# Kernel tuning notes

Hardware: AMD Instinct MI355X
Metric: run time of the kernel (lower is better)

The kernel has to match this reference:

```python
import jax, jax.numpy as jnp
import numpy as np

N, M, D = 16384, 1024, 32


def setup_inputs() -> dict:
    key = jax.random.key(0)
    k1, k2 = jax.random.split(key)
    x = jax.random.normal(k1, (N, D), dtype=jnp.float32)
    centers = jax.random.normal(k2, (M, D), dtype=jnp.float32)
    sigma = jnp.ones((M, D), dtype=jnp.float32)  # get_sigma_ones(s=1.0)
    return {"x": x, "centers": centers, "sigma": sigma}


def reference(x, centers, sigma):
    # Gaussian RBF kernel: exp(-0.5 * delta^T invCov delta) / sqrt((2pi)^D det(S))
    d = x.shape[1]
    s2 = sigma ** 2  # (M, D)
    # invCovMat: inverse of per-center diagonal covariance -> diag(1/s2)
    invCov = jnp.eye(d, dtype=x.dtype) * (1.0 / s2)[:, :, None]  # (M, D, D)
    # denom: sqrt((2pi)^D * prod(s2))
    k = (2.0 * np.pi) ** d  # python float, safe for D=32 in f32
    detS = jnp.sqrt(jnp.asarray(k, x.dtype) * jnp.prod(s2, axis=1))  # (M,)
    delta = x[:, None, :] - centers[None, :, :]  # (N, M, D)
    # batched (1,D) @ (D,D) per (n,m) pair, then elementwise * delta and reduce
    q = jnp.einsum('nmd,mde->nme', delta, invCov)  # (N, M, D)
    X = jnp.sum(q * delta, axis=2)  # (N, M) squared Mahalanobis distance
    return jnp.exp(-0.5 * X) / detS[None, :]  # (N, M)
```

## Files before the change

kernel.cpp:

```cpp
#include <hip/hip_runtime.h>


#define N_  16384
#define M_  1024
#define D_  32
#define NT  64
#define BLK 256

__global__ __launch_bounds__(BLK) void rbf_kernel(
    const float* __restrict__ x, const float* __restrict__ centers,
    const float* __restrict__ sigma, float* __restrict__ out)
{
    const int tid = threadIdx.x;
    const int m   = blockIdx.x * BLK + tid;
    const int n0  = blockIdx.y * NT;

    __shared__ float4 xs4 [NT * D_ / 4];
    __shared__ float4 x2s4[NT * D_ / 4];

    {
        const float4* xg = (const float4*)(x + (size_t)n0 * D_);
        #pragma unroll
        for (int i = tid; i < NT * D_ / 4; i += BLK) {
            float4 v = xg[i];
            xs4[i]  = v;
            x2s4[i] = make_float4(v.x * v.x, v.y * v.y, v.z * v.z, v.w * v.w);
        }
    }

    float w[D_], a[D_];
    float b = 0.0f, ld = 0.0f;
    #pragma unroll
    for (int d = 0; d < D_; ++d) {
        float s  = sigma[(size_t)m * D_ + d];
        float c  = centers[(size_t)m * D_ + d];
        float s2 = s * s;
        float wi = 1.0f / s2;
        float ai = c * wi;
        w[d] = wi;
        a[d] = ai;
        b  = fmaf(c, ai, b);
        ld += log2f(s2);
    }
    const float L2E = 1.4426950408889634f;
    const float LOG2_2PI = 2.6514961294723187f;
    const float c0 = fmaf(-0.5f * L2E, b, -0.5f * (D_ * LOG2_2PI + ld));

    __syncthreads();

    for (int i = 0; i < NT; ++i) {
        const float4* xr  = &xs4 [i * (D_ / 4)];
        const float4* x2r = &x2s4[i * (D_ / 4)];
        float s1a = 0.f, s1b = 0.f, s2a = 0.f, s2b = 0.f;
        #pragma unroll
        for (int k = 0; k < D_ / 4; ++k) {
            float4 xv = xr[k];
            float4 q  = x2r[k];
            s2a = fmaf(xv.x, a[4*k+0], s2a);
            s2b = fmaf(xv.y, a[4*k+1], s2b);
            s2a = fmaf(xv.z, a[4*k+2], s2a);
            s2b = fmaf(xv.w, a[4*k+3], s2b);
            s1a = fmaf(q.x,  w[4*k+0], s1a);
            s1b = fmaf(q.y,  w[4*k+1], s1b);
            s1a = fmaf(q.z,  w[4*k+2], s1a);
            s1b = fmaf(q.w,  w[4*k+3], s1b);
        }
        float S1 = s1a + s1b;
        float S2 = s2a + s2b;
        float f  = fmaf(L2E, S2, fmaf(-0.5f * L2E, S1, c0));
        out[(size_t)(n0 + i) * M_ + m] = __builtin_amdgcn_exp2f(f);
    }
}

extern "C" void kernel_launch(void* const* d_in, const int* in_sizes, int n_in,
                              void* d_out, int out_size, void* d_ws, size_t ws_size,
                              hipStream_t stream) {
    const float* x = (const float*)d_in[0];
    const float* c = (const float*)d_in[1];
    const float* s = (const float*)d_in[2];
    float* out = (float*)d_out;
    dim3 grid(M_ / BLK, N_ / NT);
    rbf_kernel<<<grid, BLK, 0, stream>>>(x, c, s, out);
}
```

Before: 111.4 us.

## Add uniform-sigma fast path using precomputed row norms and packed FMAs

Each thread checks at runtime whether its center's sigma is uniform across dimensions. When every lane in the wavefront agrees, it drops the per-dimension x² term and uses a precomputed per-row ||x||² (stored in shared memory) with a single scalar weight. The dot product then runs on 2-wide vector FMAs, and x is read directly from global memory (wave-uniform loads) instead of from shared tiles. A general fallback path keeps correctness for non-uniform sigma, at the cost of extra code and a runtime check.

```diff
diff --git a/kernel.cpp b/kernel.cpp
--- a/kernel.cpp
+++ b/kernel.cpp
@@ -7,6 +7,8 @@
 #define NT  64
 #define BLK 256
 
+typedef float v2f __attribute__((ext_vector_type(2)));
+
 __global__ __launch_bounds__(BLK) void rbf_kernel(
     const float* __restrict__ x, const float* __restrict__ centers,
     const float* __restrict__ sigma, float* __restrict__ out)
@@ -15,60 +17,99 @@
     const int m   = blockIdx.x * BLK + tid;
     const int n0  = blockIdx.y * NT;
 
-    __shared__ float4 xs4 [NT * D_ / 4];
-    __shared__ float4 x2s4[NT * D_ / 4];
+    __shared__ float r2s[NT];
 
+    if (tid < NT) {
+        const float4* xr = (const float4*)(x + (size_t)(n0 + tid) * D_);
+        float a0 = 0.f, a1 = 0.f, a2 = 0.f, a3 = 0.f;
+        #pragma unroll
+        for (int k = 0; k < D_ / 4; ++k) {
+            float4 v = xr[k];
+            a0 = fmaf(v.x, v.x, a0); a1 = fmaf(v.y, v.y, a1);
+            a2 = fmaf(v.z, v.z, a2); a3 = fmaf(v.w, v.w, a3);
+        }
+        r2s[tid] = (a0 + a1) + (a2 + a3);
+    }
+    __syncthreads();
+
+    const float L2E      = 1.4426950408889634f;
+    const float LOG2_2PI = 2.6514961294723187f;
+
+    float s2_0 = 0.f, ld = 0.f;
+    bool uf = true;
     {
-        const float4* xg = (const float4*)(x + (size_t)n0 * D_);
+        const float* sg = sigma + (size_t)m * D_;
         #pragma unroll
-        for (int i = tid; i < NT * D_ / 4; i += BLK) {
-            float4 v = xg[i];
-            xs4[i]  = v;
-            x2s4[i] = make_float4(v.x * v.x, v.y * v.y, v.z * v.z, v.w * v.w);
+        for (int d = 0; d < D_; ++d) {
+            float s  = sg[d];
+            float s2 = s * s;
+            if (d == 0) s2_0 = s2;
+            uf = uf && (s2 == s2_0);
+            ld += log2f(s2);
         }
     }
 
-    float w[D_], a[D_];
-    float b = 0.0f, ld = 0.0f;
-    #pragma unroll
-    for (int d = 0; d < D_; ++d) {
-        float s  = sigma[(size_t)m * D_ + d];
-        float c  = centers[(size_t)m * D_ + d];
-        float s2 = s * s;
-        float wi = 1.0f / s2;
-        float ai = c * wi;
-        w[d] = wi;
-        a[d] = ai;
-        b  = fmaf(c, ai, b);
-        ld += log2f(s2);
-    }
-    const float L2E = 1.4426950408889634f;
-    const float LOG2_2PI = 2.6514961294723187f;
-    const float c0 = fmaf(-0.5f * L2E, b, -0.5f * (D_ * LOG2_2PI + ld));
+    if (__all((int)uf)) {
+        const float w0 = 1.0f / s2_0;
+        v2f av[D_ / 2];
+        float b = 0.f;
+        {
+            const v2f* cg = (const v2f*)(centers + (size_t)m * D_);
+            #pragma unroll
+            for (int j = 0; j < D_ / 2; ++j) {
+                v2f c = cg[j];
+                v2f a = c * w0;
+                av[j] = a;
+                b = fmaf(c.x, a.x, b);
+                b = fmaf(c.y, a.y, b);
+            }
+        }
+        const float c0 = fmaf(-0.5f * L2E, b, -0.5f * (D_ * LOG2_2PI + ld));
+        const float q  = -0.5f * L2E * w0;
 
-    __syncthreads();
-
-    for (int i = 0; i < NT; ++i) {
-        const float4* xr  = &xs4 [i * (D_ / 4)];
-        const float4* x2r = &x2s4[i * (D_ / 4)];
-        float s1a = 0.f, s1b = 0.f, s2a = 0.f, s2b = 0.f;
-        #pragma unroll
-        for (int k = 0; k < D_ / 4; ++k) {
-            float4 xv = xr[k];
-            float4 q  = x2r[k];
-            s2a = fmaf(xv.x, a[4*k+0], s2a);
-            s2b = fmaf(xv.y, a[4*k+1], s2b);
-            s2a = fmaf(xv.z, a[4*k+2], s2a);
-            s2b = fmaf(xv.w, a[4*k+3], s2b);
-            s1a = fmaf(q.x,  w[4*k+0], s1a);
-            s1b = fmaf(q.y,  w[4*k+1], s1b);
-            s1a = fmaf(q.z,  w[4*k+2], s1a);
-            s1b = fmaf(q.w,  w[4*k+3], s1b);
+        for (int i = 0; i < NT; ++i) {
+            const v2f* xr = (const v2f*)(x + (size_t)(n0 + i) * D_);
+            v2f acc0 = {0.f, 0.f}, acc1 = {0.f, 0.f};
+            v2f acc2 = {0.f, 0.f}, acc3 = {0.f, 0.f};
+            #pragma unroll
+            for (int j = 0; j < D_ / 2; j += 4) {
+                acc0 += xr[j + 0] * av[j + 0];
+                acc1 += xr[j + 1] * av[j + 1];
+                acc2 += xr[j + 2] * av[j + 2];
+                acc3 += xr[j + 3] * av[j + 3];
+            }
+            v2f s = (acc0 + acc1) + (acc2 + acc3);
+            float S2 = s.x + s.y;
+            float f  = fmaf(L2E, S2, fmaf(q, r2s[i], c0));
+            out[(size_t)(n0 + i) * M_ + m] = __builtin_amdgcn_exp2f(f);
         }
-        float S1 = s1a + s1b;
-        float S2 = s2a + s2b;
-        float f  = fmaf(L2E, S2, fmaf(-0.5f * L2E, S1, c0));
-        out[(size_t)(n0 + i) * M_ + m] = __builtin_amdgcn_exp2f(f);
+    } else {
+        float wv[D_], cv[D_];
+        {
+            const float* sg = sigma   + (size_t)m * D_;
+            const float* cg = centers + (size_t)m * D_;
+            #pragma unroll
+            for (int d = 0; d < D_; ++d) {
+                float s = sg[d];
+                wv[d] = 1.0f / (s * s);
+                cv[d] = cg[d];
+            }
+        }
+        const float c0 = -0.5f * (D_ * LOG2_2PI + ld);
+        for (int i = 0; i < NT; ++i) {
+            const float* xr = x + (size_t)(n0 + i) * D_;
+            float a0 = 0.f, a1 = 0.f;
+            #pragma unroll
+            for (int d = 0; d < D_; d += 2) {
+                float t0 = xr[d]     - cv[d];
+                float t1 = xr[d + 1] - cv[d + 1];
+                a0 = fmaf(t0 * wv[d],     t0, a0);
+                a1 = fmaf(t1 * wv[d + 1], t1, a1);
+            }
+            float X = a0 + a1;
+            float f = fmaf(-0.5f * L2E, X, c0);
+            out[(size_t)(n0 + i) * M_ + m] = __builtin_amdgcn_exp2f(f);
+        }
     }
 }
 
```

Result: faster. 96.05 us (-13.8%).
